# Optimization experiments

Hardware: AMD Instinct MI355X
Metric: run time of the kernel (lower is better)

The kernel has to match this reference:

```python
import jax, jax.numpy as jnp
import numpy as np

N = 50000    # nodes
E = 800000   # edges (avg degree 16)
IN, H, OUT = 128, 16, 300


def setup_inputs() -> dict:
    key = jax.random.key(0)
    ks = jax.random.split(key, 8)
    x = jax.random.normal(ks[0], (N, IN), jnp.float32)
    edge_index = jax.random.randint(ks[1], (2, E), 0, N, jnp.int32)

    def w(k, i, o):
        return jax.random.normal(k, (i, o), jnp.float32) / np.float32(np.sqrt(i))

    return dict(
        x=x, edge_index=edge_index,
        W1=w(ks[2], IN, H), b1=jnp.zeros((H,), jnp.float32),
        Wl1=w(ks[3], IN, H), bl1=jnp.zeros((H,), jnp.float32),
        W2=w(ks[4], H, H), b2=jnp.zeros((H,), jnp.float32),
        Wl2=w(ks[5], H, H), bl2=jnp.zeros((H,), jnp.float32),
        Wo=w(ks[6], H, OUT), bo=jnp.zeros((OUT,), jnp.float32),
    )


def gcn_conv(x, W, b, src, dst, n):
    """PyG GCNConv: x@W, symmetric norm with self-loops, scatter-add, + bias."""
    h = x @ W                                    # [N, F_out]
    ones = jnp.ones(src.shape[0], h.dtype)
    deg = jax.ops.segment_sum(ones, dst, num_segments=n) + 1.0  # +1 self-loop
    dinv = jax.lax.rsqrt(deg)                    # deg >= 1, safe
    norm = dinv[src] * dinv[dst]                 # [E]
    agg = jax.ops.segment_sum(h[src] * norm[:, None], dst, num_segments=n)
    agg = agg + h * (dinv * dinv)[:, None]       # self-loop message
    return agg + b


def reference(x, edge_index, W1, b1, Wl1, bl1, W2, b2, Wl2, bl2, Wo, bo):
    src, dst = edge_index[0], edge_index[1]
    n = x.shape[0]
    # layer 1: conv.relu + skip linear  (dropout p=0 / inference -> identity)
    h = jax.nn.relu(gcn_conv(x, W1, b1, src, dst, n)) + (x @ Wl1 + bl1)
    # layer 2
    h = jax.nn.relu(gcn_conv(h, W2, b2, src, dst, n)) + (h @ Wl2 + bl2)
    # output conv + log_softmax over classes
    out = gcn_conv(h, Wo, bo, src, dst, n)
    return jax.nn.log_softmax(out, axis=1)
```

## Files before the change

kernel.cpp:

```cpp
#include <hip/hip_runtime.h>
#include <hip/hip_bf16.h>

#define NN   50000
#define EE   800000
#define INF_ 128
#define HH   16
#define OUTC 300

#define NB   196
#define CAP  4608
#define CHK  4096
#define GB_  196

#define W1_OFF   0
#define WL1_OFF  2048
#define B1_OFF   4096
#define BL1_OFF  4112
#define W2_OFF   4128
#define WL2_OFF  4384
#define B2_OFF   4640
#define BL2_OFF  4656
#define WO_OFF   4672
#define BO_OFF   9472
#define WC_TOT   9772

__device__ __forceinline__ float bfu2f(unsigned short u) {
    return __uint_as_float(((unsigned)u) << 16);
}
__device__ __forceinline__ unsigned short f2bfu(float f) {
    __hip_bfloat16 h = __float2bfloat16(f);
    return *reinterpret_cast<unsigned short*>(&h);
}
__device__ __forceinline__ unsigned packbf(float lo, float hi) {
    return (unsigned)f2bfu(lo) | ((unsigned)f2bfu(hi) << 16);
}
__device__ __forceinline__ float cvt1(const void* p, int i, int flag) {
    return flag ? ((const float*)p)[i] : bfu2f(((const unsigned short*)p)[i]);
}

__global__ __launch_bounds__(256) void convert_kernel(
    const void* __restrict__ W1, const void* __restrict__ Wl1,
    const void* __restrict__ b1, const void* __restrict__ bl1,
    const void* __restrict__ W2, const void* __restrict__ Wl2,
    const void* __restrict__ b2, const void* __restrict__ bl2,
    const void* __restrict__ Wo, const void* __restrict__ bo,
    const unsigned* __restrict__ xw, int* __restrict__ flagp,
    int* __restrict__ gcur, float* __restrict__ wc)
{
    __shared__ int shits;
    int tid = threadIdx.x;
    if (tid == 0) shits = 0;
    __syncthreads();
    unsigned w = xw[tid];
    float lo = __uint_as_float(w << 16);
    if (!(fabsf(lo) < 1e4f)) atomicAdd(&shits, 1);
    __syncthreads();
    const int flag = (shits > 8) ? 1 : 0;

    if (blockIdx.x == 0) {
        if (tid == 0) flagp[0] = flag;
        if (tid < NB) gcur[tid] = 0;
    }

    int t = blockIdx.x * 256 + tid;
    if (t >= WC_TOT) return;
    float v;
    if      (t < WL1_OFF) v = cvt1(W1,  t - W1_OFF,  flag);
    else if (t < B1_OFF)  v = cvt1(Wl1, t - WL1_OFF, flag);
    else if (t < BL1_OFF) v = cvt1(b1,  t - B1_OFF,  flag);
    else if (t < W2_OFF)  v = cvt1(bl1, t - BL1_OFF, flag);
    else if (t < WL2_OFF) v = cvt1(W2,  t - W2_OFF,  flag);
    else if (t < B2_OFF)  v = cvt1(Wl2, t - WL2_OFF, flag);
    else if (t < BL2_OFF) v = cvt1(b2,  t - B2_OFF,  flag);
    else if (t < WO_OFF)  v = cvt1(bl2, t - BL2_OFF, flag);
    else if (t < BO_OFF)  v = cvt1(Wo,  t - WO_OFF,  flag);
    else                  v = cvt1(bo,  t - BO_OFF,  flag);
    wc[t] = v;
}

__global__ __launch_bounds__(256) void bplace_kernel(
    const int* __restrict__ src, const int* __restrict__ dst,
    int* __restrict__ gcur, uint2* __restrict__ gpairs)
{
    __shared__ uint2 raw[CHK];
    __shared__ uint2 srt[CHK];
    __shared__ unsigned char bid[CHK];
    __shared__ int cnt[NB];
    __shared__ int loff[NB];
    __shared__ int cur2[NB];
    __shared__ int gbase[NB];
    __shared__ int sc[256];

    int tid = threadIdx.x;
    int e0 = blockIdx.x * CHK;
    int n = min(CHK, EE - e0);
    if (n <= 0) return;
    for (int t = tid; t < NB; t += 256) cnt[t] = 0;
    __syncthreads();

    for (int j = tid; j < n; j += 256) {
        unsigned s = (unsigned)src[e0 + j];
        unsigned d = (unsigned)dst[e0 + j];
        raw[j] = make_uint2(s, d);
        atomicAdd(&cnt[d >> 8], 1);
    }
    __syncthreads();

    int v = (tid < NB) ? cnt[tid] : 0;
    sc[tid] = v;
    __syncthreads();
    for (int d = 1; d < 256; d <<= 1) {
        int u = (tid >= d) ? sc[tid - d] : 0;
        __syncthreads();
        sc[tid] += u;
        __syncthreads();
    }
    if (tid < NB) { loff[tid] = sc[tid] - v; cur2[tid] = sc[tid] - v; }
    __syncthreads();

    for (int j = tid; j < n; j += 256) {
        uint2 p = raw[j];
        int b = (int)(p.y >> 8);
        int pos = atomicAdd(&cur2[b], 1);
        srt[pos] = p;
        bid[pos] = (unsigned char)b;
    }
    __syncthreads();

    if (tid < NB) {
        int c = cnt[tid];
        gbase[tid] = c ? atomicAdd(&gcur[tid], c) : 0;
    }
    __syncthreads();

    for (int j = tid; j < n; j += 256) {
        int b = bid[j];
        int p = gbase[b] + (j - loff[b]);
        if (p < CAP) gpairs[(size_t)b * CAP + p] = srt[j];
    }
}

__global__ __launch_bounds__(256) void cplace_kernel(
    const uint2* __restrict__ gpairs, const int* __restrict__ gcur,
    int* __restrict__ off, float* __restrict__ dinv, int* __restrict__ csr_src)
{
    __shared__ uint2 pl[CAP];
    __shared__ int sc[256];
    __shared__ int ncnt[256];
    __shared__ int nscan[256];
    __shared__ int ncur[256];
    int b = blockIdx.x, t = threadIdx.x;

    int bv = (t < NB) ? gcur[t] : 0;
    sc[t] = bv;
    __syncthreads();
    for (int d = 1; d < 256; d <<= 1) {
        int u = (t >= d) ? sc[t - d] : 0;
        __syncthreads();
        sc[t] += u;
        __syncthreads();
    }
    __shared__ int gb_s;
    if (t == b) gb_s = sc[t] - bv;
    if (b == 0 && t == 0) off[NN] = EE;
    ncnt[t] = 0;
    __syncthreads();
    int gb = gb_s;

    int c = min(gcur[b], CAP);
    int nb = b << 8;
    for (int j = t; j < c; j += 256) pl[j] = gpairs[(size_t)b * CAP + j];
    __syncthreads();

    for (int j = t; j < c; j += 256) atomicAdd(&ncnt[pl[j].y & 255], 1);
    __syncthreads();

    int v = ncnt[t];
    nscan[t] = v;
    __syncthreads();
    for (int d = 1; d < 256; d <<= 1) {
        int u = (t >= d) ? nscan[t - d] : 0;
        __syncthreads();
        nscan[t] += u;
        __syncthreads();
    }
    int excl = nscan[t] - v;
    ncur[t] = excl;

    int node = nb + t;
    if (node < NN) {
        off[node] = gb + excl;
        dinv[node] = rsqrtf((float)v + 1.0f);
    }
    __syncthreads();

    for (int j = t; j < c; j += 256) {
        uint2 p = pl[j];
        int d = (int)(p.y & 255);
        int pos = atomicAdd(&ncur[d], 1);
        csr_src[gb + pos] = (int)p.x;
    }
}

__global__ __launch_bounds__(256) void lin1_kernel(
    const void* __restrict__ xp, const float* __restrict__ wc,
    const float* __restrict__ dinv, const int* __restrict__ flagp,
    unsigned short* __restrict__ A, unsigned short* __restrict__ B)
{
    __shared__ float2 sWL[INF_ * HH];
    __shared__ float sb[HH];
    for (int t = threadIdx.x; t < INF_ * HH; t += 256)
        sWL[t] = make_float2(wc[W1_OFF + t], wc[WL1_OFF + t]);
    if (threadIdx.x < HH) sb[threadIdx.x] = wc[BL1_OFF + threadIdx.x];
    __syncthreads();

    int i = blockIdx.x * 256 + threadIdx.x;
    if (i >= NN) return;
    const int flag = flagp[0];

    float a[HH], l[HH];
#pragma unroll
    for (int f = 0; f < HH; f++) { a[f] = 0.f; l[f] = 0.f; }

    for (int k0 = 0; k0 < INF_ / 8; k0++) {
        float xv[8];
        if (flag) {
            const float4* xr = (const float4*)((const float*)xp + (size_t)i * INF_);
            float4 r0 = xr[k0 * 2], r1 = xr[k0 * 2 + 1];
            xv[0] = r0.x; xv[1] = r0.y; xv[2] = r0.z; xv[3] = r0.w;
            xv[4] = r1.x; xv[5] = r1.y; xv[6] = r1.z; xv[7] = r1.w;
        } else {
            const uint4* xr = (const uint4*)((const unsigned short*)xp + (size_t)i * INF_);
            uint4 v = xr[k0];
            unsigned uu[4] = { v.x, v.y, v.z, v.w };
#pragma unroll
            for (int q = 0; q < 4; q++) {
                xv[q * 2]     = __uint_as_float(uu[q] << 16);
                xv[q * 2 + 1] = __uint_as_float(uu[q] & 0xffff0000u);
            }
        }
#pragma unroll
        for (int j = 0; j < 8; j++) {
            float xj = xv[j];
            int k = k0 * 8 + j;
#pragma unroll
            for (int f = 0; f < HH; f++) {
                float2 wv = sWL[k * HH + f];
                a[f] = fmaf(xj, wv.x, a[f]);
                l[f] = fmaf(xj, wv.y, l[f]);
            }
        }
    }
    float di = dinv[i];
    unsigned pa[8], pb[8];
#pragma unroll
    for (int h = 0; h < 8; h++) {
        pa[h] = packbf(a[2 * h] * di, a[2 * h + 1] * di);
        pb[h] = packbf(l[2 * h] + sb[2 * h], l[2 * h + 1] + sb[2 * h + 1]);
    }
    uint4* Ar = (uint4*)(A + (size_t)i * HH);
    uint4* Br = (uint4*)(B + (size_t)i * HH);
    Ar[0] = make_uint4(pa[0], pa[1], pa[2], pa[3]);
    Ar[1] = make_uint4(pa[4], pa[5], pa[6], pa[7]);
    Br[0] = make_uint4(pb[0], pb[1], pb[2], pb[3]);
    Br[1] = make_uint4(pb[4], pb[5], pb[6], pb[7]);
}

__global__ __launch_bounds__(256) void gather_combine_kernel(
    const int* __restrict__ off, const int* __restrict__ csr,
    const float* __restrict__ dinv, const unsigned short* __restrict__ X,
    unsigned short* __restrict__ Y, const float* __restrict__ bias, int mode)
{
    int lane = threadIdx.x & 63;
    int w = (blockIdx.x * 256 + threadIdx.x) >> 6;
    int n = lane >> 4, j = lane & 15;
    int node = w * 4 + n;
    int s0 = off[node], s1 = off[node + 1];
    int deg = s1 - s0;

    int wmax = deg;
    wmax = max(wmax, __shfl_xor(wmax, 16));
    wmax = max(wmax, __shfl_xor(wmax, 32));

    const uint2* X4 = (const uint2*)X;
    float a0 = 0.f, a1 = 0.f, a2 = 0.f, a3 = 0.f;
    int eh = j >> 2, q = j & 3;

    for (int base = 0; base < wmax; base += 16) {
        int p = s0 + base + j;
        int sj = (p < s1) ? csr[p] : 0;
#pragma unroll
        for (int r = 0; r < 4; r++) {
            int e = r * 4 + eh;
            int se = __shfl(sj, (n << 4) + e);
            bool val = (base + e) < deg;
            uint2 v = X4[(size_t)(val ? se : node) * 4 + q];
            if (val) {
                a0 += __uint_as_float(v.x << 16);
                a1 += __uint_as_float(v.x & 0xffff0000u);
                a2 += __uint_as_float(v.y << 16);
                a3 += __uint_as_float(v.y & 0xffff0000u);
            }
        }
    }
#pragma unroll
    for (int m = 4; m <= 8; m <<= 1) {
        a0 += __shfl_xor(a0, m);
        a1 += __shfl_xor(a1, m);
        a2 += __shfl_xor(a2, m);
        a3 += __shfl_xor(a3, m);
    }
    if (eh == 0) {
        float di = dinv[node];
        uint2 xv = X4[(size_t)node * 4 + q];
        float x0 = __uint_as_float(xv.x << 16);
        float x1 = __uint_as_float(xv.x & 0xffff0000u);
        float x2 = __uint_as_float(xv.y << 16);
        float x3 = __uint_as_float(xv.y & 0xffff0000u);
        float o0, o1, o2, o3;
        if (mode == 2) {
            o0 = di * (a0 + x0); o1 = di * (a1 + x1);
            o2 = di * (a2 + x2); o3 = di * (a3 + x3);
        } else {
            uint2 yv = ((const uint2*)Y)[(size_t)node * 4 + q];
            float y0 = __uint_as_float(yv.x << 16);
            float y1 = __uint_as_float(yv.x & 0xffff0000u);
            float y2 = __uint_as_float(yv.y << 16);
            float y3 = __uint_as_float(yv.y & 0xffff0000u);
            o0 = fmaxf(di * (a0 + x0) + bias[q * 4 + 0], 0.f) + y0;
            o1 = fmaxf(di * (a1 + x1) + bias[q * 4 + 1], 0.f) + y1;
            o2 = fmaxf(di * (a2 + x2) + bias[q * 4 + 2], 0.f) + y2;
            o3 = fmaxf(di * (a3 + x3) + bias[q * 4 + 3], 0.f) + y3;
            if (mode) { o0 *= di; o1 *= di; o2 *= di; o3 *= di; }
        }
        ((uint2*)Y)[(size_t)node * 4 + q] = make_uint2(packbf(o0, o1), packbf(o2, o3));
    }
}

__global__ __launch_bounds__(256) void lin2_kernel(
    unsigned short* __restrict__ B, const float* __restrict__ wc,
    const float* __restrict__ dinv, unsigned short* __restrict__ A)
{
    __shared__ float2 sWL[HH * HH];
    __shared__ float sb[HH];
    for (int t = threadIdx.x; t < HH * HH; t += 256)
        sWL[t] = make_float2(wc[W2_OFF + t], wc[WL2_OFF + t]);
    if (threadIdx.x < HH) sb[threadIdx.x] = wc[BL2_OFF + threadIdx.x];
    __syncthreads();

    int i = blockIdx.x * 256 + threadIdx.x;
    if (i >= NN) return;

    float z[HH];
    const uint4* br = (const uint4*)(B + (size_t)i * HH);
    uint4 r0 = br[0], r1 = br[1];
    unsigned uu[8] = { r0.x, r0.y, r0.z, r0.w, r1.x, r1.y, r1.z, r1.w };
#pragma unroll
    for (int h = 0; h < 8; h++) {
        z[2 * h]     = __uint_as_float(uu[h] << 16);
        z[2 * h + 1] = __uint_as_float(uu[h] & 0xffff0000u);
    }
    float a[HH], l[HH];
#pragma unroll
    for (int f = 0; f < HH; f++) { a[f] = 0.f; l[f] = 0.f; }
#pragma unroll
    for (int k = 0; k < HH; k++) {
        float zk = z[k];
#pragma unroll
        for (int f = 0; f < HH; f++) {
            float2 wv = sWL[k * HH + f];
            a[f] = fmaf(zk, wv.x, a[f]);
            l[f] = fmaf(zk, wv.y, l[f]);
        }
    }
    float di = dinv[i];
    unsigned pa[8], pb[8];
#pragma unroll
    for (int h = 0; h < 8; h++) {
        pa[h] = packbf(a[2 * h] * di, a[2 * h + 1] * di);
        pb[h] = packbf(l[2 * h] + sb[2 * h], l[2 * h + 1] + sb[2 * h + 1]);
    }
    uint4* Ar = (uint4*)(A + (size_t)i * HH);
    uint4* Br = (uint4*)(B + (size_t)i * HH);
    Ar[0] = make_uint4(pa[0], pa[1], pa[2], pa[3]);
    Ar[1] = make_uint4(pa[4], pa[5], pa[6], pa[7]);
    Br[0] = make_uint4(pb[0], pb[1], pb[2], pb[3]);
    Br[1] = make_uint4(pb[4], pb[5], pb[6], pb[7]);
}

__global__ __launch_bounds__(256) void final_kernel(
    const unsigned short* __restrict__ Z, const float* __restrict__ wc,
    const int* __restrict__ flagp, void* __restrict__ outp)
{
    __shared__ float sW[HH * OUTC];
    __shared__ float sbb[OUTC];
    for (int t = threadIdx.x; t < HH * OUTC; t += 256) sW[t] = wc[WO_OFF + t];
    for (int t = threadIdx.x; t < OUTC; t += 256)      sbb[t] = wc[BO_OFF + t];
    __syncthreads();

    const int flag = flagp[0];
    int wave = threadIdx.x >> 6, lane = threadIdx.x & 63;
    int i0 = blockIdx.x * 16 + wave * 4;

    float zf[4];
#pragma unroll
    for (int n = 0; n < 4; n++) zf[n] = bfu2f(Z[(size_t)(i0 + n) * HH + (lane & 15)]);

    float y[4][5];
#pragma unroll
    for (int jj = 0; jj < 5; jj++) {
        int j = lane + jj * 64;
        float b = (j < OUTC) ? sbb[j] : 0.f;
#pragma unroll
        for (int n = 0; n < 4; n++) y[n][jj] = b;
    }

#pragma unroll
    for (int k = 0; k < HH; k++) {
        float zb[4];
#pragma unroll
        for (int n = 0; n < 4; n++) zb[n] = __shfl(zf[n], k);
#pragma unroll
        for (int jj = 0; jj < 5; jj++) {
            int j = lane + jj * 64;
            float w = (j < OUTC) ? sW[k * OUTC + j] : 0.f;
#pragma unroll
            for (int n = 0; n < 4; n++) y[n][jj] = fmaf(zb[n], w, y[n][jj]);
        }
    }

#pragma unroll
    for (int n = 0; n < 4; n++) {
        float m = -1e30f;
#pragma unroll
        for (int jj = 0; jj < 5; jj++) {
            int j = lane + jj * 64;
            if (j < OUTC) m = fmaxf(m, y[n][jj]);
        }
#pragma unroll
        for (int o = 32; o > 0; o >>= 1) m = fmaxf(m, __shfl_xor(m, o));
        float s = 0.f;
#pragma unroll
        for (int jj = 0; jj < 5; jj++) {
            int j = lane + jj * 64;
            if (j < OUTC) s += __expf(y[n][jj] - m);
        }
#pragma unroll
        for (int o = 32; o > 0; o >>= 1) s += __shfl_xor(s, o);
        float lse = m + __logf(s);
#pragma unroll
        for (int jj = 0; jj < 5; jj++) {
            int j = lane + jj * 64;
            if (j < OUTC) {
                float v = y[n][jj] - lse;
                size_t ofs = (size_t)(i0 + n) * OUTC + j;
                if (flag) ((float*)outp)[ofs] = v;
                else      ((__hip_bfloat16*)outp)[ofs] = __float2bfloat16(v);
            }
        }
    }
}

extern "C" void kernel_launch(void* const* d_in, const int* in_sizes, int n_in,
                              void* d_out, int out_size, void* d_ws, size_t ws_size,
                              hipStream_t stream) {
    const void* x   = d_in[0];
    const int*  ei  = (const int*)d_in[1];
    const void* W1  = d_in[2];
    const void* b1  = d_in[3];
    const void* Wl1 = d_in[4];
    const void* bl1 = d_in[5];
    const void* W2  = d_in[6];
    const void* b2  = d_in[7];
    const void* Wl2 = d_in[8];
    const void* bl2 = d_in[9];
    const void* Wo  = d_in[10];
    const void* bo  = d_in[11];

    const int* srcp = ei;
    const int* dstp = ei + EE;

    char* wsb = (char*)d_ws;
    int*   flag    = (int*)wsb;
    float* wc      = (float*)(wsb + 4 * 16);
    int*   gcur    = (int*)(wsb + 4 * 10000);
    int*   off     = (int*)(wsb + 4 * 10400);
    int*   csr_src = (int*)(wsb + 4 * 60416);
    float* dinv    = (float*)(wsb + 4 * 860416);
    uint2* gpairs  = (uint2*)(wsb + 4 * 910416);
    unsigned short* A = (unsigned short*)(wsb + 4 * 2716752);
    unsigned short* B = (unsigned short*)(wsb + 4 * 3116752);

    const int gN  = (NN + 255) / 256;
    const int gG4 = (NN / 4 * 64) / 256;
    const int gW  = (WC_TOT + 255) / 256;

    convert_kernel<<<gW, 256, 0, stream>>>(W1, Wl1, b1, bl1, W2, Wl2, b2, bl2,
                                           Wo, bo, (const unsigned*)x, flag, gcur, wc);

    bplace_kernel<<<GB_, 256, 0, stream>>>(srcp, dstp, gcur, gpairs);
    cplace_kernel<<<NB, 256, 0, stream>>>(gpairs, gcur, off, dinv, csr_src);

    lin1_kernel<<<gN, 256, 0, stream>>>(x, wc, dinv, flag, A, B);
    gather_combine_kernel<<<gG4, 256, 0, stream>>>(off, csr_src, dinv, A, B, wc + B1_OFF, 0);

    lin2_kernel<<<gN, 256, 0, stream>>>(B, wc, dinv, A);
    gather_combine_kernel<<<gG4, 256, 0, stream>>>(off, csr_src, dinv, A, B, wc + B2_OFF, 1);

    gather_combine_kernel<<<gG4, 256, 0, stream>>>(off, csr_src, dinv, B, A, wc + B2_OFF, 2);

    final_kernel<<<gG4, 256, 0, stream>>>(A, wc, flag, d_out);
}
```

Before: 226.7 us.

## Fuse layer-1 gather with lin2 and final gather with output projection

```diff
diff --git a/kernel.cpp b/kernel.cpp
--- a/kernel.cpp
+++ b/kernel.cpp
@@ -37,6 +37,8 @@
 __device__ __forceinline__ float cvt1(const void* p, int i, int flag) {
     return flag ? ((const float*)p)[i] : bfu2f(((const unsigned short*)p)[i]);
 }
+__device__ __forceinline__ float louf(unsigned u) { return __uint_as_float(u << 16); }
+__device__ __forceinline__ float hiuf(unsigned u) { return __uint_as_float(u & 0xffff0000u); }
 
 __global__ __launch_bounds__(256) void convert_kernel(
     const void* __restrict__ W1, const void* __restrict__ Wl1,
@@ -296,10 +298,8 @@
             bool val = (base + e) < deg;
             uint2 v = X4[(size_t)(val ? se : node) * 4 + q];
             if (val) {
-                a0 += __uint_as_float(v.x << 16);
-                a1 += __uint_as_float(v.x & 0xffff0000u);
-                a2 += __uint_as_float(v.y << 16);
-                a3 += __uint_as_float(v.y & 0xffff0000u);
+                a0 += louf(v.x); a1 += hiuf(v.x);
+                a2 += louf(v.y); a3 += hiuf(v.y);
             }
         }
     }
@@ -313,149 +313,206 @@
     if (eh == 0) {
         float di = dinv[node];
         uint2 xv = X4[(size_t)node * 4 + q];
-        float x0 = __uint_as_float(xv.x << 16);
-        float x1 = __uint_as_float(xv.x & 0xffff0000u);
-        float x2 = __uint_as_float(xv.y << 16);
-        float x3 = __uint_as_float(xv.y & 0xffff0000u);
-        float o0, o1, o2, o3;
-        if (mode == 2) {
-            o0 = di * (a0 + x0); o1 = di * (a1 + x1);
-            o2 = di * (a2 + x2); o3 = di * (a3 + x3);
-        } else {
-            uint2 yv = ((const uint2*)Y)[(size_t)node * 4 + q];
-            float y0 = __uint_as_float(yv.x << 16);
-            float y1 = __uint_as_float(yv.x & 0xffff0000u);
-            float y2 = __uint_as_float(yv.y << 16);
-            float y3 = __uint_as_float(yv.y & 0xffff0000u);
-            o0 = fmaxf(di * (a0 + x0) + bias[q * 4 + 0], 0.f) + y0;
-            o1 = fmaxf(di * (a1 + x1) + bias[q * 4 + 1], 0.f) + y1;
-            o2 = fmaxf(di * (a2 + x2) + bias[q * 4 + 2], 0.f) + y2;
-            o3 = fmaxf(di * (a3 + x3) + bias[q * 4 + 3], 0.f) + y3;
-            if (mode) { o0 *= di; o1 *= di; o2 *= di; o3 *= di; }
-        }
+        uint2 yv = ((const uint2*)Y)[(size_t)node * 4 + q];
+        float y0 = louf(yv.x), y1 = hiuf(yv.x), y2 = louf(yv.y), y3 = hiuf(yv.y);
+        float o0 = fmaxf(di * (a0 + louf(xv.x)) + bias[q * 4 + 0], 0.f) + y0;
+        float o1 = fmaxf(di * (a1 + hiuf(xv.x)) + bias[q * 4 + 1], 0.f) + y1;
+        float o2 = fmaxf(di * (a2 + louf(xv.y)) + bias[q * 4 + 2], 0.f) + y2;
+        float o3 = fmaxf(di * (a3 + hiuf(xv.y)) + bias[q * 4 + 3], 0.f) + y3;
+        if (mode) { o0 *= di; o1 *= di; o2 *= di; o3 *= di; }
         ((uint2*)Y)[(size_t)node * 4 + q] = make_uint2(packbf(o0, o1), packbf(o2, o3));
     }
 }
 
-__global__ __launch_bounds__(256) void lin2_kernel(
-    unsigned short* __restrict__ B, const float* __restrict__ wc,
-    const float* __restrict__ dinv, unsigned short* __restrict__ A)
-{
-    __shared__ float2 sWL[HH * HH];
-    __shared__ float sb[HH];
-    for (int t = threadIdx.x; t < HH * HH; t += 256)
-        sWL[t] = make_float2(wc[W2_OFF + t], wc[WL2_OFF + t]);
-    if (threadIdx.x < HH) sb[threadIdx.x] = wc[BL2_OFF + threadIdx.x];
-    __syncthreads();
-
-    int i = blockIdx.x * 256 + threadIdx.x;
-    if (i >= NN) return;
-
-    float z[HH];
-    const uint4* br = (const uint4*)(B + (size_t)i * HH);
-    uint4 r0 = br[0], r1 = br[1];
-    unsigned uu[8] = { r0.x, r0.y, r0.z, r0.w, r1.x, r1.y, r1.z, r1.w };
-#pragma unroll
-    for (int h = 0; h < 8; h++) {
-        z[2 * h]     = __uint_as_float(uu[h] << 16);
-        z[2 * h + 1] = __uint_as_float(uu[h] & 0xffff0000u);
-    }
-    float a[HH], l[HH];
-#pragma unroll
-    for (int f = 0; f < HH; f++) { a[f] = 0.f; l[f] = 0.f; }
+__global__ __launch_bounds__(256) void gather_lin2_kernel(
+    const int* __restrict__ off, const int* __restrict__ csr,
+    const float* __restrict__ dinv, const unsigned short* __restrict__ X,
+    const unsigned short* __restrict__ Yin, const float* __restrict__ wc,
+    unsigned short* __restrict__ A2, unsigned short* __restrict__ B2)
+{
+    int lane = threadIdx.x & 63;
+    int w = (blockIdx.x * 256 + threadIdx.x) >> 6;
+    int n = lane >> 4, j = lane & 15;
+    int node = w * 4 + n;
+    int s0 = off[node], s1 = off[node + 1];
+    int deg = s1 - s0;
+
+    int wmax = deg;
+    wmax = max(wmax, __shfl_xor(wmax, 16));
+    wmax = max(wmax, __shfl_xor(wmax, 32));
+
+    const uint2* X4 = (const uint2*)X;
+    float a0 = 0.f, a1 = 0.f, a2 = 0.f, a3 = 0.f;
+    int eh = j >> 2, q = j & 3;
+
+    for (int base = 0; base < wmax; base += 16) {
+        int p = s0 + base + j;
+        int sj = (p < s1) ? csr[p] : 0;
+#pragma unroll
+        for (int r = 0; r < 4; r++) {
+            int e = r * 4 + eh;
+            int se = __shfl(sj, (n << 4) + e);
+            bool val = (base + e) < deg;
+            uint2 v = X4[(size_t)(val ? se : node) * 4 + q];
+            if (val) {
+                a0 += louf(v.x); a1 += hiuf(v.x);
+                a2 += louf(v.y); a3 += hiuf(v.y);
+            }
+        }
+    }
+#pragma unroll
+    for (int m = 4; m <= 8; m <<= 1) {
+        a0 += __shfl_xor(a0, m);
+        a1 += __shfl_xor(a1, m);
+        a2 += __shfl_xor(a2, m);
+        a3 += __shfl_xor(a3, m);
+    }
+    float di = dinv[node];
+    uint2 xv = X4[(size_t)node * 4 + q];
+    uint2 yv = ((const uint2*)Yin)[(size_t)node * 4 + q];
+    float4 bq = ((const float4*)(wc + B1_OFF))[q];
+    float o0 = fmaxf(di * (a0 + louf(xv.x)) + bq.x, 0.f) + louf(yv.x);
+    float o1 = fmaxf(di * (a1 + hiuf(xv.x)) + bq.y, 0.f) + hiuf(yv.x);
+    float o2 = fmaxf(di * (a2 + louf(xv.y)) + bq.z, 0.f) + louf(yv.y);
+    float o3 = fmaxf(di * (a3 + hiuf(xv.y)) + bq.w, 0.f) + hiuf(yv.y);
+
+    int f = j;
+    float a = 0.f, l = 0.f;
 #pragma unroll
     for (int k = 0; k < HH; k++) {
-        float zk = z[k];
-#pragma unroll
-        for (int f = 0; f < HH; f++) {
-            float2 wv = sWL[k * HH + f];
-            a[f] = fmaf(zk, wv.x, a[f]);
-            l[f] = fmaf(zk, wv.y, l[f]);
-        }
-    }
-    float di = dinv[i];
-    unsigned pa[8], pb[8];
-#pragma unroll
-    for (int h = 0; h < 8; h++) {
-        pa[h] = packbf(a[2 * h] * di, a[2 * h + 1] * di);
-        pb[h] = packbf(l[2 * h] + sb[2 * h], l[2 * h + 1] + sb[2 * h + 1]);
-    }
-    uint4* Ar = (uint4*)(A + (size_t)i * HH);
-    uint4* Br = (uint4*)(B + (size_t)i * HH);
-    Ar[0] = make_uint4(pa[0], pa[1], pa[2], pa[3]);
-    Ar[1] = make_uint4(pa[4], pa[5], pa[6], pa[7]);
-    Br[0] = make_uint4(pb[0], pb[1], pb[2], pb[3]);
-    Br[1] = make_uint4(pb[4], pb[5], pb[6], pb[7]);
-}
-
-__global__ __launch_bounds__(256) void final_kernel(
-    const unsigned short* __restrict__ Z, const float* __restrict__ wc,
-    const int* __restrict__ flagp, void* __restrict__ outp)
-{
-    __shared__ float sW[HH * OUTC];
-    __shared__ float sbb[OUTC];
-    for (int t = threadIdx.x; t < HH * OUTC; t += 256) sW[t] = wc[WO_OFF + t];
-    for (int t = threadIdx.x; t < OUTC; t += 256)      sbb[t] = wc[BO_OFF + t];
-    __syncthreads();
-
+        int srcl = (lane & 48) + (k >> 2);
+        float hk;
+        if      ((k & 3) == 0) hk = __shfl(o0, srcl);
+        else if ((k & 3) == 1) hk = __shfl(o1, srcl);
+        else if ((k & 3) == 2) hk = __shfl(o2, srcl);
+        else                   hk = __shfl(o3, srcl);
+        a = fmaf(hk, wc[W2_OFF  + k * HH + f], a);
+        l = fmaf(hk, wc[WL2_OFF + k * HH + f], l);
+    }
+    A2[(size_t)node * HH + f] = f2bfu(a * di);
+    B2[(size_t)node * HH + f] = f2bfu(l + wc[BL2_OFF + f]);
+}
+
+__global__ __launch_bounds__(256) void gather_final_kernel(
+    const int* __restrict__ off, const int* __restrict__ csr,
+    const float* __restrict__ dinv, const unsigned short* __restrict__ X,
+    const float* __restrict__ wc, const int* __restrict__ flagp,
+    void* __restrict__ outp)
+{
+    int lane = threadIdx.x & 63;
+    int w = (blockIdx.x * 256 + threadIdx.x) >> 6;
+    int n = lane >> 4, j = lane & 15;
+    int node = w * 4 + n;
+    int s0 = off[node], s1 = off[node + 1];
+    int deg = s1 - s0;
+
+    int wmax = deg;
+    wmax = max(wmax, __shfl_xor(wmax, 16));
+    wmax = max(wmax, __shfl_xor(wmax, 32));
+
+    const uint2* X4 = (const uint2*)X;
+    float a0 = 0.f, a1 = 0.f, a2 = 0.f, a3 = 0.f;
+    int eh = j >> 2, q = j & 3;
+
+    for (int base = 0; base < wmax; base += 16) {
+        int p = s0 + base + j;
+        int sj = (p < s1) ? csr[p] : 0;
+#pragma unroll
+        for (int r = 0; r < 4; r++) {
+            int e = r * 4 + eh;
+            int se = __shfl(sj, (n << 4) + e);
+            bool val = (base + e) < deg;
+            uint2 v = X4[(size_t)(val ? se : node) * 4 + q];
+            if (val) {
+                a0 += louf(v.x); a1 += hiuf(v.x);
+                a2 += louf(v.y); a3 += hiuf(v.y);
+            }
+        }
+    }
+#pragma unroll
+    for (int m = 4; m <= 8; m <<= 1) {
+        a0 += __shfl_xor(a0, m);
+        a1 += __shfl_xor(a1, m);
+        a2 += __shfl_xor(a2, m);
+        a3 += __shfl_xor(a3, m);
+    }
+    float di = dinv[node];
+    uint2 xv = X4[(size_t)node * 4 + q];
+    float o0 = di * (a0 + louf(xv.x));
+    float o1 = di * (a1 + hiuf(xv.x));
+    float o2 = di * (a2 + louf(xv.y));
+    float o3 = di * (a3 + hiuf(xv.y));
+
+    const float* Wo = wc + WO_OFF;
+    const float* bo = wc + BO_OFF;
     const int flag = flagp[0];
-    int wave = threadIdx.x >> 6, lane = threadIdx.x & 63;
-    int i0 = blockIdx.x * 16 + wave * 4;
-
-    float zf[4];
-#pragma unroll
-    for (int n = 0; n < 4; n++) zf[n] = bfu2f(Z[(size_t)(i0 + n) * HH + (lane & 15)]);
-
-    float y[4][5];
-#pragma unroll
-    for (int jj = 0; jj < 5; jj++) {
-        int j = lane + jj * 64;
-        float b = (j < OUTC) ? sbb[j] : 0.f;
-#pragma unroll
-        for (int n = 0; n < 4; n++) y[n][jj] = b;
+    int g = j;
+    const bool v4 = (g < 11);
+
+    float4 y4[5];
+#pragma unroll
+    for (int c = 0; c < 5; c++) {
+        if (c < 4 || v4) y4[c] = ((const float4*)bo)[g + 16 * c];
+        else             y4[c] = make_float4(0.f, 0.f, 0.f, 0.f);
     }
 
 #pragma unroll
     for (int k = 0; k < HH; k++) {
-        float zb[4];
-#pragma unroll
-        for (int n = 0; n < 4; n++) zb[n] = __shfl(zf[n], k);
-#pragma unroll
-        for (int jj = 0; jj < 5; jj++) {
-            int j = lane + jj * 64;
-            float w = (j < OUTC) ? sW[k * OUTC + j] : 0.f;
-#pragma unroll
-            for (int n = 0; n < 4; n++) y[n][jj] = fmaf(zb[n], w, y[n][jj]);
-        }
-    }
-
-#pragma unroll
-    for (int n = 0; n < 4; n++) {
-        float m = -1e30f;
-#pragma unroll
-        for (int jj = 0; jj < 5; jj++) {
-            int j = lane + jj * 64;
-            if (j < OUTC) m = fmaxf(m, y[n][jj]);
-        }
-#pragma unroll
-        for (int o = 32; o > 0; o >>= 1) m = fmaxf(m, __shfl_xor(m, o));
-        float s = 0.f;
-#pragma unroll
-        for (int jj = 0; jj < 5; jj++) {
-            int j = lane + jj * 64;
-            if (j < OUTC) s += __expf(y[n][jj] - m);
-        }
-#pragma unroll
-        for (int o = 32; o > 0; o >>= 1) s += __shfl_xor(s, o);
-        float lse = m + __logf(s);
-#pragma unroll
-        for (int jj = 0; jj < 5; jj++) {
-            int j = lane + jj * 64;
-            if (j < OUTC) {
-                float v = y[n][jj] - lse;
-                size_t ofs = (size_t)(i0 + n) * OUTC + j;
-                if (flag) ((float*)outp)[ofs] = v;
-                else      ((__hip_bfloat16*)outp)[ofs] = __float2bfloat16(v);
+        int srcl = (lane & 48) + (k >> 2);
+        float zk;
+        if      ((k & 3) == 0) zk = __shfl(o0, srcl);
+        else if ((k & 3) == 1) zk = __shfl(o1, srcl);
+        else if ((k & 3) == 2) zk = __shfl(o2, srcl);
+        else                   zk = __shfl(o3, srcl);
+        const float4* wr = (const float4*)(Wo + k * OUTC);
+#pragma unroll
+        for (int c = 0; c < 5; c++) {
+            if (c < 4 || v4) {
+                float4 wq = wr[g + 16 * c];
+                y4[c].x = fmaf(zk, wq.x, y4[c].x);
+                y4[c].y = fmaf(zk, wq.y, y4[c].y);
+                y4[c].z = fmaf(zk, wq.z, y4[c].z);
+                y4[c].w = fmaf(zk, wq.w, y4[c].w);
+            }
+        }
+    }
+
+    float m = fmaxf(fmaxf(y4[0].x, y4[0].y), fmaxf(y4[0].z, y4[0].w));
+#pragma unroll
+    for (int c = 1; c < 4; c++)
+        m = fmaxf(m, fmaxf(fmaxf(y4[c].x, y4[c].y), fmaxf(y4[c].z, y4[c].w)));
+    if (v4) m = fmaxf(m, fmaxf(fmaxf(y4[4].x, y4[4].y), fmaxf(y4[4].z, y4[4].w)));
+#pragma unroll
+    for (int o_ = 1; o_ <= 8; o_ <<= 1) m = fmaxf(m, __shfl_xor(m, o_));
+
+    float s = 0.f;
+#pragma unroll
+    for (int c = 0; c < 4; c++)
+        s += __expf(y4[c].x - m) + __expf(y4[c].y - m)
+           + __expf(y4[c].z - m) + __expf(y4[c].w - m);
+    if (v4) s += __expf(y4[4].x - m) + __expf(y4[4].y - m)
+               + __expf(y4[4].z - m) + __expf(y4[4].w - m);
+#pragma unroll
+    for (int o_ = 1; o_ <= 8; o_ <<= 1) s += __shfl_xor(s, o_);
+    float lse = m + __logf(s);
+
+    if (flag) {
+        float* orow = (float*)outp + (size_t)node * OUTC;
+#pragma unroll
+        for (int c = 0; c < 5; c++) {
+            if (c < 4 || v4) {
+                *(float4*)(orow + 4 * (g + 16 * c)) = make_float4(
+                    y4[c].x - lse, y4[c].y - lse, y4[c].z - lse, y4[c].w - lse);
+            }
+        }
+    } else {
+        unsigned short* orow = (unsigned short*)outp + (size_t)node * OUTC;
+#pragma unroll
+        for (int c = 0; c < 5; c++) {
+            if (c < 4 || v4) {
+                *(uint2*)(orow + 4 * (g + 16 * c)) = make_uint2(
+                    packbf(y4[c].x - lse, y4[c].y - lse),
+                    packbf(y4[c].z - lse, y4[c].w - lse));
             }
         }
     }
@@ -488,8 +545,10 @@
     int*   csr_src = (int*)(wsb + 4 * 60416);
     float* dinv    = (float*)(wsb + 4 * 860416);
     uint2* gpairs  = (uint2*)(wsb + 4 * 910416);
-    unsigned short* A = (unsigned short*)(wsb + 4 * 2716752);
-    unsigned short* B = (unsigned short*)(wsb + 4 * 3116752);
+    unsigned short* A  = (unsigned short*)(wsb + 4 * 2716752);
+    unsigned short* B  = (unsigned short*)(wsb + 4 * 3116752);
+    unsigned short* A2 = (unsigned short*)(wsb + 4 * 3516752);
+    unsigned short* B2 = (unsigned short*)(wsb + 4 * 3916752);
 
     const int gN  = (NN + 255) / 256;
     const int gG4 = (NN / 4 * 64) / 256;
@@ -502,12 +561,9 @@
     cplace_kernel<<<NB, 256, 0, stream>>>(gpairs, gcur, off, dinv, csr_src);
 
     lin1_kernel<<<gN, 256, 0, stream>>>(x, wc, dinv, flag, A, B);
-    gather_combine_kernel<<<gG4, 256, 0, stream>>>(off, csr_src, dinv, A, B, wc + B1_OFF, 0);
-
-    lin2_kernel<<<gN, 256, 0, stream>>>(B, wc, dinv, A);
-    gather_combine_kernel<<<gG4, 256, 0, stream>>>(off, csr_src, dinv, A, B, wc + B2_OFF, 1);
-
-    gather_combine_kernel<<<gG4, 256, 0, stream>>>(off, csr_src, dinv, B, A, wc + B2_OFF, 2);
-
-    final_kernel<<<gG4, 256, 0, stream>>>(A, wc, flag, d_out);
-}
+    gather_lin2_kernel<<<gG4, 256, 0, stream>>>(off, csr_src, dinv, A, B, wc, A2, B2);
+
+    gather_combine_kernel<<<gG4, 256, 0, stream>>>(off, csr_src, dinv, A2, B2, wc + B2_OFF, 1);
+
+    gather_final_kernel<<<gG4, 256, 0, stream>>>(off, csr_src, dinv, B2, wc, flag, d_out);
+}
```

After: 270.4 us. +19.3%, slower.
